# Kernel optimization log

Hardware: AMD Instinct MI355X
Metric: run time of the kernel (lower is better)

The kernel has to match this reference:

```python
import jax, jax.numpy as jnp
import numpy as np

# HistogramQuantizer(percentile=99.99, gamma=0.99, n_bits=8, eps=0.0, act_decay=0.01), training mode
PERCENTILE = 99.99 / 100.0
GAMMA = 0.99
Q_MAX = float(2 ** (8 - 1) - 1)  # 127.0
EPS = 0.0
CLAMP_INIT = 100.0  # registered buffer initial value


def setup_inputs() -> dict:
    key = jax.random.key(0)
    x = jax.random.normal(key, (4, 4096, 4096), dtype=jnp.float32)
    return {"x": x}


def reference(x):
    x_abs = jnp.abs(x)
    # --- training-path percentile via full sort (quantile_from_sorted) ---
    flat = jnp.sort(x_abs.ravel())
    n = flat.size  # static
    k = int(round(PERCENTILE * n)) - 1
    clamp_value = flat[k]
    # EMA buffer update (side state; returned so the sort is not dead code)
    new_buffer = CLAMP_INIT * GAMMA + clamp_value * (1.0 - GAMMA)
    # --- fake quantization (Quantizer.forward with q_max=Q_MAX) ---
    # note: x_max/clamp_value only affects the backward mask, not the forward math
    scale = Q_MAX / jnp.maximum(jnp.max(x_abs), EPS)
    out = jnp.clip(jnp.round(x * scale), -Q_MAX, Q_MAX) / scale
    return out, new_buffer
```

## Files before the change

### kernel.cpp

```cpp
#include <hip/hip_runtime.h>
#include <math.h>

#define WS_MAXBITS 0
#define WS_COUNT   1
#define WS_SELBIN  2
#define WS_RANK    3
#define WS_HIST    4
#define HIST_WORDS 4096
#define WS_CAND    4128

extern "C" __global__ void __launch_bounds__(256)
k_max_hist(const float* __restrict__ x, long n, unsigned int* __restrict__ ws) {
    __shared__ unsigned int lhist[HIST_WORDS];
    __shared__ unsigned int wred[4];
    for (int i = threadIdx.x; i < HIST_WORDS; i += 256) lhist[i] = 0;
    __syncthreads();

    long n4 = n >> 2;
    const float4* x4 = (const float4*)x;
    unsigned int mymax = 0;
    long stride = (long)gridDim.x * 256;
    for (long i = (long)blockIdx.x * 256 + threadIdx.x; i < n4; i += stride) {
        float4 v = x4[i];
        unsigned int a0 = __float_as_uint(fabsf(v.x));
        unsigned int a1 = __float_as_uint(fabsf(v.y));
        unsigned int a2 = __float_as_uint(fabsf(v.z));
        unsigned int a3 = __float_as_uint(fabsf(v.w));
        mymax = max(mymax, max(max(a0, a1), max(a2, a3)));
        atomicAdd(&lhist[a0 >> 20], 1u);
        atomicAdd(&lhist[a1 >> 20], 1u);
        atomicAdd(&lhist[a2 >> 20], 1u);
        atomicAdd(&lhist[a3 >> 20], 1u);
    }
    if (blockIdx.x == 0 && threadIdx.x < (int)(n & 3)) {
        unsigned int a = __float_as_uint(fabsf(x[n4 * 4 + threadIdx.x]));
        atomicAdd(&ws[WS_HIST + (a >> 20)], 1u);
        atomicMax(&ws[WS_MAXBITS], a);
    }

    for (int off = 32; off > 0; off >>= 1)
        mymax = max(mymax, __shfl_down(mymax, off, 64));
    int lane = threadIdx.x & 63, wid = threadIdx.x >> 6;
    if (lane == 0) wred[wid] = mymax;
    __syncthreads();
    if (threadIdx.x == 0) {
        unsigned int m = max(max(wred[0], wred[1]), max(wred[2], wred[3]));
        atomicMax(&ws[WS_MAXBITS], m);
    }
    for (int i = threadIdx.x; i < HIST_WORDS; i += 256) {
        unsigned int c = lhist[i];
        if (c) atomicAdd(&ws[WS_HIST + i], c);
    }
}

extern "C" __global__ void __launch_bounds__(256)
k_scan(unsigned int* __restrict__ ws, long k) {
    __shared__ unsigned long long partial[256];
    const unsigned int* hist = ws + WS_HIST;
    int base = threadIdx.x * (HIST_WORDS / 256);
    unsigned long long s = 0;
    for (int i = 0; i < 16; i++) s += hist[base + i];
    partial[threadIdx.x] = s;
    __syncthreads();
    if (threadIdx.x == 0) {
        unsigned long long acc = 0;
        long bin = -1;
        unsigned long long before = 0;
        for (int t = 0; t < 256; t++) {
            unsigned long long ps = partial[t];
            if (bin < 0 && acc + ps > (unsigned long long)k) {
                unsigned long long a2 = acc;
                for (int i = 0; i < 16; i++) {
                    unsigned int c = hist[t * 16 + i];
                    if (a2 + c > (unsigned long long)k) { bin = t * 16 + i; before = a2; break; }
                    a2 += c;
                }
            }
            acc += ps;
        }
        ws[WS_SELBIN] = (unsigned int)bin;
        ws[WS_RANK]   = (unsigned int)((unsigned long long)k - before);
    }
}

extern "C" __global__ void __launch_bounds__(256)
k_quant(const float* __restrict__ x, float* __restrict__ out, long n,
        unsigned int* __restrict__ ws, unsigned int cap) {
    float xmax = __uint_as_float(ws[WS_MAXBITS]);
    unsigned int selbin = ws[WS_SELBIN];
    float scale = 127.0f / xmax;
    float inv = 1.0f / scale;
    unsigned int* cand = ws + WS_CAND;

    long n4 = n >> 2;
    const float4* x4 = (const float4*)x;
    float4* out4 = (float4*)out;
    long stride = (long)gridDim.x * 256;
    for (long i = (long)blockIdx.x * 256 + threadIdx.x; i < n4; i += stride) {
        float4 v = x4[i];
        float4 r;
        r.x = fminf(fmaxf(rintf(v.x * scale), -127.0f), 127.0f) * inv;
        r.y = fminf(fmaxf(rintf(v.y * scale), -127.0f), 127.0f) * inv;
        r.z = fminf(fmaxf(rintf(v.z * scale), -127.0f), 127.0f) * inv;
        r.w = fminf(fmaxf(rintf(v.w * scale), -127.0f), 127.0f) * inv;
        out4[i] = r;
        unsigned int a0 = __float_as_uint(fabsf(v.x));
        unsigned int a1 = __float_as_uint(fabsf(v.y));
        unsigned int a2 = __float_as_uint(fabsf(v.z));
        unsigned int a3 = __float_as_uint(fabsf(v.w));
        if ((a0 >> 20) == selbin) { unsigned int p = atomicAdd(&ws[WS_COUNT], 1u); if (p < cap) cand[p] = a0; }
        if ((a1 >> 20) == selbin) { unsigned int p = atomicAdd(&ws[WS_COUNT], 1u); if (p < cap) cand[p] = a1; }
        if ((a2 >> 20) == selbin) { unsigned int p = atomicAdd(&ws[WS_COUNT], 1u); if (p < cap) cand[p] = a2; }
        if ((a3 >> 20) == selbin) { unsigned int p = atomicAdd(&ws[WS_COUNT], 1u); if (p < cap) cand[p] = a3; }
    }
    if (blockIdx.x == 0 && threadIdx.x < (int)(n & 3)) {
        long i = n4 * 4 + threadIdx.x;
        float v = x[i];
        out[i] = fminf(fmaxf(rintf(v * scale), -127.0f), 127.0f) * inv;
        unsigned int a = __float_as_uint(fabsf(v));
        if ((a >> 20) == selbin) { unsigned int p = atomicAdd(&ws[WS_COUNT], 1u); if (p < cap) cand[p] = a; }
    }
}

extern "C" __global__ void __launch_bounds__(256)
k_select(unsigned int* __restrict__ ws, float* __restrict__ out_last, unsigned int cap) {
    __shared__ unsigned int hist[1024];
    __shared__ unsigned int s_b1, s_j2;
    unsigned int c = ws[WS_COUNT]; if (c > cap) c = cap;
    unsigned int j = ws[WS_RANK];
    unsigned int selbin = ws[WS_SELBIN];
    const unsigned int* cand = ws + WS_CAND;

    for (int i = threadIdx.x; i < 1024; i += 256) hist[i] = 0;
    __syncthreads();
    for (unsigned int i = threadIdx.x; i < c; i += 256)
        atomicAdd(&hist[(cand[i] >> 10) & 1023], 1u);
    __syncthreads();
    if (threadIdx.x == 0) {
        unsigned int acc = 0, b1 = 1023;
        for (int b = 0; b < 1024; b++) {
            unsigned int h = hist[b];
            if (acc + h > j) { b1 = (unsigned int)b; break; }
            acc += h;
        }
        s_b1 = b1; s_j2 = j - acc;
    }
    __syncthreads();
    unsigned int pref = (selbin << 10) | s_b1;
    unsigned int j2 = s_j2;
    for (int i = threadIdx.x; i < 1024; i += 256) hist[i] = 0;
    __syncthreads();
    for (unsigned int i = threadIdx.x; i < c; i += 256) {
        unsigned int u = cand[i];
        if ((u >> 10) == pref) atomicAdd(&hist[u & 1023], 1u);
    }
    __syncthreads();
    if (threadIdx.x == 0) {
        unsigned int acc = 0, b2 = 1023;
        for (int b = 0; b < 1024; b++) {
            unsigned int h = hist[b];
            if (acc + h > j2) { b2 = (unsigned int)b; break; }
            acc += h;
        }
        float clampv = __uint_as_float((pref << 10) | b2);
        out_last[0] = (float)(100.0 * 0.99 + (double)clampv * 0.01);
    }
}

extern "C" void kernel_launch(void* const* d_in, const int* in_sizes, int n_in,
                              void* d_out, int out_size, void* d_ws, size_t ws_size,
                              hipStream_t stream) {
    const float* x = (const float*)d_in[0];
    long n = (long)in_sizes[0];
    float* out = (float*)d_out;
    unsigned int* ws = (unsigned int*)d_ws;

    long k = (long)llround((99.99 / 100.0) * (double)n) - 1;
    if (k < 0) k = 0;
    if (k >= n) k = n - 1;

    long avail = (long)(ws_size / 4) - WS_CAND;
    if (avail < 0) avail = 0;
    if (avail > (1L << 22)) avail = (1L << 22);
    unsigned int cap = (unsigned int)avail;

    size_t hdr = (size_t)(WS_HIST + HIST_WORDS) * sizeof(unsigned int);
    if (hdr > ws_size) hdr = ws_size;
    hipMemsetAsync(d_ws, 0, hdr, stream);

    const int blocks = 4096;
    k_max_hist<<<blocks, 256, 0, stream>>>(x, n, ws);
    k_scan<<<1, 256, 0, stream>>>(ws, k);
    k_quant<<<blocks, 256, 0, stream>>>(x, out, n, ws, cap);
    k_select<<<1, 256, 0, stream>>>(ws, out + n, cap);
}
```

Before: 661.6 us.

## Replace global atomics with per-block max and LDS candidate buffers, unroll loops

```diff
diff --git a/kernel.cpp b/kernel.cpp
--- a/kernel.cpp
+++ b/kernel.cpp
@@ -2,12 +2,17 @@
 #include <math.h>
 
 #define WS_MAXBITS 0
-#define WS_COUNT   1
-#define WS_SELBIN  2
-#define WS_RANK    3
+#define WS_SELBIN  1
+#define WS_RANK    2
 #define WS_HIST    4
 #define HIST_WORDS 4096
-#define WS_CAND    4128
+#define WS_BMAX    4100
+#define WS_CNT     5124
+#define WS_CAND    6160
+#define NBLK       1024
+#define CAP        256
+
+typedef float floatx4 __attribute__((ext_vector_type(4)));
 
 extern "C" __global__ void __launch_bounds__(256)
 k_max_hist(const float* __restrict__ x, long n, unsigned int* __restrict__ ws) {
@@ -20,7 +25,30 @@
     const float4* x4 = (const float4*)x;
     unsigned int mymax = 0;
     long stride = (long)gridDim.x * 256;
-    for (long i = (long)blockIdx.x * 256 + threadIdx.x; i < n4; i += stride) {
+    long i = (long)blockIdx.x * 256 + threadIdx.x;
+    for (; i + stride < n4; i += 2 * stride) {
+        float4 v0 = x4[i];
+        float4 v1 = x4[i + stride];
+        unsigned int a0 = __float_as_uint(fabsf(v0.x));
+        unsigned int a1 = __float_as_uint(fabsf(v0.y));
+        unsigned int a2 = __float_as_uint(fabsf(v0.z));
+        unsigned int a3 = __float_as_uint(fabsf(v0.w));
+        unsigned int b0 = __float_as_uint(fabsf(v1.x));
+        unsigned int b1 = __float_as_uint(fabsf(v1.y));
+        unsigned int b2 = __float_as_uint(fabsf(v1.z));
+        unsigned int b3 = __float_as_uint(fabsf(v1.w));
+        mymax = max(mymax, max(max(a0, a1), max(a2, a3)));
+        mymax = max(mymax, max(max(b0, b1), max(b2, b3)));
+        atomicAdd(&lhist[a0 >> 20], 1u);
+        atomicAdd(&lhist[a1 >> 20], 1u);
+        atomicAdd(&lhist[a2 >> 20], 1u);
+        atomicAdd(&lhist[a3 >> 20], 1u);
+        atomicAdd(&lhist[b0 >> 20], 1u);
+        atomicAdd(&lhist[b1 >> 20], 1u);
+        atomicAdd(&lhist[b2 >> 20], 1u);
+        atomicAdd(&lhist[b3 >> 20], 1u);
+    }
+    for (; i < n4; i += stride) {
         float4 v = x4[i];
         unsigned int a0 = __float_as_uint(fabsf(v.x));
         unsigned int a1 = __float_as_uint(fabsf(v.y));
@@ -34,8 +62,8 @@
     }
     if (blockIdx.x == 0 && threadIdx.x < (int)(n & 3)) {
         unsigned int a = __float_as_uint(fabsf(x[n4 * 4 + threadIdx.x]));
-        atomicAdd(&ws[WS_HIST + (a >> 20)], 1u);
-        atomicMax(&ws[WS_MAXBITS], a);
+        mymax = max(mymax, a);
+        atomicAdd(&lhist[a >> 20], 1u);
     }
 
     for (int off = 32; off > 0; off >>= 1)
@@ -44,25 +72,37 @@
     if (lane == 0) wred[wid] = mymax;
     __syncthreads();
     if (threadIdx.x == 0) {
-        unsigned int m = max(max(wred[0], wred[1]), max(wred[2], wred[3]));
-        atomicMax(&ws[WS_MAXBITS], m);
-    }
-    for (int i = threadIdx.x; i < HIST_WORDS; i += 256) {
-        unsigned int c = lhist[i];
-        if (c) atomicAdd(&ws[WS_HIST + i], c);
+        ws[WS_BMAX + blockIdx.x] =
+            max(max(wred[0], wred[1]), max(wred[2], wred[3]));
+    }
+    unsigned int rot = (blockIdx.x * 1297u) & (HIST_WORDS - 1);
+    for (int idx = threadIdx.x; idx < HIST_WORDS; idx += 256) {
+        unsigned int bin = (idx + rot) & (HIST_WORDS - 1);
+        unsigned int c = lhist[bin];
+        if (c) atomicAdd(&ws[WS_HIST + bin], c);
     }
 }
 
 extern "C" __global__ void __launch_bounds__(256)
 k_scan(unsigned int* __restrict__ ws, long k) {
     __shared__ unsigned long long partial[256];
+    __shared__ unsigned int mred[256];
     const unsigned int* hist = ws + WS_HIST;
+
+    unsigned int m = 0;
+    for (int s = threadIdx.x; s < NBLK; s += 256) m = max(m, ws[WS_BMAX + s]);
+    mred[threadIdx.x] = m;
+
     int base = threadIdx.x * (HIST_WORDS / 256);
     unsigned long long s = 0;
     for (int i = 0; i < 16; i++) s += hist[base + i];
     partial[threadIdx.x] = s;
     __syncthreads();
     if (threadIdx.x == 0) {
+        unsigned int mm = 0;
+        for (int t = 0; t < 256; t++) mm = max(mm, mred[t]);
+        ws[WS_MAXBITS] = mm;
+
         unsigned long long acc = 0;
         long bin = -1;
         unsigned long long before = 0;
@@ -85,56 +125,99 @@
 
 extern "C" __global__ void __launch_bounds__(256)
 k_quant(const float* __restrict__ x, float* __restrict__ out, long n,
-        unsigned int* __restrict__ ws, unsigned int cap) {
+        unsigned int* __restrict__ ws) {
+    __shared__ unsigned int lbuf[CAP];
+    __shared__ unsigned int lcnt;
+    if (threadIdx.x == 0) lcnt = 0;
+    __syncthreads();
+
     float xmax = __uint_as_float(ws[WS_MAXBITS]);
     unsigned int selbin = ws[WS_SELBIN];
     float scale = 127.0f / xmax;
     float inv = 1.0f / scale;
-    unsigned int* cand = ws + WS_CAND;
 
     long n4 = n >> 2;
     const float4* x4 = (const float4*)x;
-    float4* out4 = (float4*)out;
+    floatx4* out4 = (floatx4*)out;
     long stride = (long)gridDim.x * 256;
-    for (long i = (long)blockIdx.x * 256 + threadIdx.x; i < n4; i += stride) {
+    long i = (long)blockIdx.x * 256 + threadIdx.x;
+    for (; i + stride < n4; i += 2 * stride) {
+        float4 v0 = x4[i];
+        float4 v1 = x4[i + stride];
+        floatx4 r0, r1;
+        r0.x = fminf(fmaxf(rintf(v0.x * scale), -127.0f), 127.0f) * inv;
+        r0.y = fminf(fmaxf(rintf(v0.y * scale), -127.0f), 127.0f) * inv;
+        r0.z = fminf(fmaxf(rintf(v0.z * scale), -127.0f), 127.0f) * inv;
+        r0.w = fminf(fmaxf(rintf(v0.w * scale), -127.0f), 127.0f) * inv;
+        r1.x = fminf(fmaxf(rintf(v1.x * scale), -127.0f), 127.0f) * inv;
+        r1.y = fminf(fmaxf(rintf(v1.y * scale), -127.0f), 127.0f) * inv;
+        r1.z = fminf(fmaxf(rintf(v1.z * scale), -127.0f), 127.0f) * inv;
+        r1.w = fminf(fmaxf(rintf(v1.w * scale), -127.0f), 127.0f) * inv;
+        __builtin_nontemporal_store(r0, &out4[i]);
+        __builtin_nontemporal_store(r1, &out4[i + stride]);
+        unsigned int a0 = __float_as_uint(fabsf(v0.x));
+        unsigned int a1 = __float_as_uint(fabsf(v0.y));
+        unsigned int a2 = __float_as_uint(fabsf(v0.z));
+        unsigned int a3 = __float_as_uint(fabsf(v0.w));
+        unsigned int b0 = __float_as_uint(fabsf(v1.x));
+        unsigned int b1 = __float_as_uint(fabsf(v1.y));
+        unsigned int b2 = __float_as_uint(fabsf(v1.z));
+        unsigned int b3 = __float_as_uint(fabsf(v1.w));
+        if ((a0 >> 20) == selbin) { unsigned int p = atomicAdd(&lcnt, 1u); if (p < CAP) lbuf[p] = a0; }
+        if ((a1 >> 20) == selbin) { unsigned int p = atomicAdd(&lcnt, 1u); if (p < CAP) lbuf[p] = a1; }
+        if ((a2 >> 20) == selbin) { unsigned int p = atomicAdd(&lcnt, 1u); if (p < CAP) lbuf[p] = a2; }
+        if ((a3 >> 20) == selbin) { unsigned int p = atomicAdd(&lcnt, 1u); if (p < CAP) lbuf[p] = a3; }
+        if ((b0 >> 20) == selbin) { unsigned int p = atomicAdd(&lcnt, 1u); if (p < CAP) lbuf[p] = b0; }
+        if ((b1 >> 20) == selbin) { unsigned int p = atomicAdd(&lcnt, 1u); if (p < CAP) lbuf[p] = b1; }
+        if ((b2 >> 20) == selbin) { unsigned int p = atomicAdd(&lcnt, 1u); if (p < CAP) lbuf[p] = b2; }
+        if ((b3 >> 20) == selbin) { unsigned int p = atomicAdd(&lcnt, 1u); if (p < CAP) lbuf[p] = b3; }
+    }
+    for (; i < n4; i += stride) {
         float4 v = x4[i];
-        float4 r;
+        floatx4 r;
         r.x = fminf(fmaxf(rintf(v.x * scale), -127.0f), 127.0f) * inv;
         r.y = fminf(fmaxf(rintf(v.y * scale), -127.0f), 127.0f) * inv;
         r.z = fminf(fmaxf(rintf(v.z * scale), -127.0f), 127.0f) * inv;
         r.w = fminf(fmaxf(rintf(v.w * scale), -127.0f), 127.0f) * inv;
-        out4[i] = r;
+        __builtin_nontemporal_store(r, &out4[i]);
         unsigned int a0 = __float_as_uint(fabsf(v.x));
         unsigned int a1 = __float_as_uint(fabsf(v.y));
         unsigned int a2 = __float_as_uint(fabsf(v.z));
         unsigned int a3 = __float_as_uint(fabsf(v.w));
-        if ((a0 >> 20) == selbin) { unsigned int p = atomicAdd(&ws[WS_COUNT], 1u); if (p < cap) cand[p] = a0; }
-        if ((a1 >> 20) == selbin) { unsigned int p = atomicAdd(&ws[WS_COUNT], 1u); if (p < cap) cand[p] = a1; }
-        if ((a2 >> 20) == selbin) { unsigned int p = atomicAdd(&ws[WS_COUNT], 1u); if (p < cap) cand[p] = a2; }
-        if ((a3 >> 20) == selbin) { unsigned int p = atomicAdd(&ws[WS_COUNT], 1u); if (p < cap) cand[p] = a3; }
+        if ((a0 >> 20) == selbin) { unsigned int p = atomicAdd(&lcnt, 1u); if (p < CAP) lbuf[p] = a0; }
+        if ((a1 >> 20) == selbin) { unsigned int p = atomicAdd(&lcnt, 1u); if (p < CAP) lbuf[p] = a1; }
+        if ((a2 >> 20) == selbin) { unsigned int p = atomicAdd(&lcnt, 1u); if (p < CAP) lbuf[p] = a2; }
+        if ((a3 >> 20) == selbin) { unsigned int p = atomicAdd(&lcnt, 1u); if (p < CAP) lbuf[p] = a3; }
     }
     if (blockIdx.x == 0 && threadIdx.x < (int)(n & 3)) {
-        long i = n4 * 4 + threadIdx.x;
-        float v = x[i];
-        out[i] = fminf(fmaxf(rintf(v * scale), -127.0f), 127.0f) * inv;
+        long t = n4 * 4 + threadIdx.x;
+        float v = x[t];
+        out[t] = fminf(fmaxf(rintf(v * scale), -127.0f), 127.0f) * inv;
         unsigned int a = __float_as_uint(fabsf(v));
-        if ((a >> 20) == selbin) { unsigned int p = atomicAdd(&ws[WS_COUNT], 1u); if (p < cap) cand[p] = a; }
-    }
-}
-
-extern "C" __global__ void __launch_bounds__(256)
-k_select(unsigned int* __restrict__ ws, float* __restrict__ out_last, unsigned int cap) {
+        if ((a >> 20) == selbin) { unsigned int p = atomicAdd(&lcnt, 1u); if (p < CAP) lbuf[p] = a; }
+    }
+    __syncthreads();
+    unsigned int c = lcnt; if (c > CAP) c = CAP;
+    unsigned int* seg = ws + WS_CAND + (unsigned int)blockIdx.x * CAP;
+    for (unsigned int e = threadIdx.x; e < c; e += 256) seg[e] = lbuf[e];
+    if (threadIdx.x == 0) ws[WS_CNT + blockIdx.x] = c;
+}
+
+extern "C" __global__ void __launch_bounds__(256)
+k_select(unsigned int* __restrict__ ws, float* __restrict__ out_last) {
     __shared__ unsigned int hist[1024];
     __shared__ unsigned int s_b1, s_j2;
-    unsigned int c = ws[WS_COUNT]; if (c > cap) c = cap;
     unsigned int j = ws[WS_RANK];
     unsigned int selbin = ws[WS_SELBIN];
-    const unsigned int* cand = ws + WS_CAND;
 
     for (int i = threadIdx.x; i < 1024; i += 256) hist[i] = 0;
     __syncthreads();
-    for (unsigned int i = threadIdx.x; i < c; i += 256)
-        atomicAdd(&hist[(cand[i] >> 10) & 1023], 1u);
+    for (int s = threadIdx.x; s < NBLK; s += 256) {
+        unsigned int c = ws[WS_CNT + s]; if (c > CAP) c = CAP;
+        const unsigned int* seg = ws + WS_CAND + (unsigned int)s * CAP;
+        for (unsigned int e = 0; e < c; e++)
+            atomicAdd(&hist[(seg[e] >> 10) & 1023], 1u);
+    }
     __syncthreads();
     if (threadIdx.x == 0) {
         unsigned int acc = 0, b1 = 1023;
@@ -150,9 +233,13 @@
     unsigned int j2 = s_j2;
     for (int i = threadIdx.x; i < 1024; i += 256) hist[i] = 0;
     __syncthreads();
-    for (unsigned int i = threadIdx.x; i < c; i += 256) {
-        unsigned int u = cand[i];
-        if ((u >> 10) == pref) atomicAdd(&hist[u & 1023], 1u);
+    for (int s = threadIdx.x; s < NBLK; s += 256) {
+        unsigned int c = ws[WS_CNT + s]; if (c > CAP) c = CAP;
+        const unsigned int* seg = ws + WS_CAND + (unsigned int)s * CAP;
+        for (unsigned int e = 0; e < c; e++) {
+            unsigned int u = seg[e];
+            if ((u >> 10) == pref) atomicAdd(&hist[u & 1023], 1u);
+        }
     }
     __syncthreads();
     if (threadIdx.x == 0) {
@@ -179,18 +266,11 @@
     if (k < 0) k = 0;
     if (k >= n) k = n - 1;
 
-    long avail = (long)(ws_size / 4) - WS_CAND;
-    if (avail < 0) avail = 0;
-    if (avail > (1L << 22)) avail = (1L << 22);
-    unsigned int cap = (unsigned int)avail;
-
-    size_t hdr = (size_t)(WS_HIST + HIST_WORDS) * sizeof(unsigned int);
-    if (hdr > ws_size) hdr = ws_size;
-    hipMemsetAsync(d_ws, 0, hdr, stream);
-
-    const int blocks = 4096;
-    k_max_hist<<<blocks, 256, 0, stream>>>(x, n, ws);
+    (void)hipMemsetAsync((char*)d_ws + WS_HIST * sizeof(unsigned int), 0,
+                         HIST_WORDS * sizeof(unsigned int), stream);
+
+    k_max_hist<<<NBLK, 256, 0, stream>>>(x, n, ws);
     k_scan<<<1, 256, 0, stream>>>(ws, k);
-    k_quant<<<blocks, 256, 0, stream>>>(x, out, n, ws, cap);
-    k_select<<<1, 256, 0, stream>>>(ws, out + n, cap);
-}
+    k_quant<<<NBLK, 256, 0, stream>>>(x, out, n, ws);
+    k_select<<<1, 256, 0, stream>>>(ws, out + n);
+}
```

Result: faster. 588.5 us (-11.0%).
